# Performance work log

Hardware: AMD Instinct MI355X
Metric: run time of the kernel (lower is better)

## Reference

```python
import jax, jax.numpy as jnp
import numpy as np

FP8_MAX = 448.0  # max finite value of float8_e4m3fn


def _fp8_quant_dequant(t, scale):
    """Per-tensor static FP8 e4m3fn quantize -> dequantize (simulated real quant)."""
    q = jnp.clip(t / scale, -FP8_MAX, FP8_MAX).astype(jnp.float8_e4m3fn)
    return q.astype(jnp.float32) * scale


def setup_inputs() -> dict:
    key = jax.random.key(0)
    k1, k2, k3 = jax.random.split(key, 3)
    M, K, N = 4096, 4096, 14336  # tokens, in_features, out_features
    x = jax.random.normal(k1, (M, K), jnp.float32)
    weight = jax.random.normal(k2, (N, K), jnp.float32) * 0.02
    bias = jax.random.normal(k3, (N,), jnp.float32) * 0.01
    # static per-tensor calibration scales (amax / fp8_max)
    input_scale = (jnp.max(jnp.abs(x)) / FP8_MAX).reshape(1)
    weight_scale = (jnp.max(jnp.abs(weight)) / FP8_MAX).reshape(1)
    return {"x": x, "weight": weight, "bias": bias,
            "input_scale": input_scale, "weight_scale": weight_scale}


def reference(x, weight, bias, input_scale, weight_scale):
    # QParamsLinear forward: statically quantize input to fp8 e4m3fn with the
    # input quantizer's per-tensor scale, dequantize the fp8 weight with its
    # per-tensor scale, run the GEMM (y = x_dq @ W_dq^T), and add bias.
    s_in = input_scale[0]
    s_w = weight_scale[0]
    x_dq = _fp8_quant_dequant(x, s_in)      # [M, K]
    w_dq = _fp8_quant_dequant(weight, s_w)  # [N, K]
    return jnp.einsum('mk,nk->mn', x_dq, w_dq) + bias[None, :]
```

## Files before the change

kernel.cpp:

```cpp
#include <hip/hip_runtime.h>
#include <stdint.h>

typedef float f32x4 __attribute__((ext_vector_type(4)));
typedef int   i32x8 __attribute__((ext_vector_type(8)));
typedef long  i64x2 __attribute__((ext_vector_type(2)));

#define FP8_MAX_V 448.0f

__device__ __forceinline__ uint32_t pack4_fp8(float a, float b, float c, float d) {
    a = fminf(fmaxf(a, -FP8_MAX_V), FP8_MAX_V);
    b = fminf(fmaxf(b, -FP8_MAX_V), FP8_MAX_V);
    c = fminf(fmaxf(c, -FP8_MAX_V), FP8_MAX_V);
    d = fminf(fmaxf(d, -FP8_MAX_V), FP8_MAX_V);
    int v = 0;
    v = __builtin_amdgcn_cvt_pk_fp8_f32(a, b, v, false);
    v = __builtin_amdgcn_cvt_pk_fp8_f32(c, d, v, true);
    return (uint32_t)v;
}

__global__ void quant_fp8_kernel(const float* __restrict__ in,
                                 uint32_t* __restrict__ out,
                                 const float* __restrict__ scale_ptr,
                                 long long n4) {
    const float s = scale_ptr[0];
    long long i = (long long)blockIdx.x * blockDim.x + threadIdx.x;
    const long long stride = (long long)gridDim.x * blockDim.x;
    const float4* in4 = (const float4*)in;
    for (; i < n4; i += stride) {
        float4 v = in4[i];
        out[i] = pack4_fp8(v.x / s, v.y / s, v.z / s, v.w / s);
    }
}

__global__ __launch_bounds__(256, 2) void gemm_mxfp8_kernel(
    const uint8_t* __restrict__ qA,
    const uint8_t* __restrict__ qB,
    const float* __restrict__ bias,
    const float* __restrict__ s_in_p,
    const float* __restrict__ s_w_p,
    float* __restrict__ C,
    int M, int N, int K) {
    __shared__ uint8_t lds[49152];

    const int tid = threadIdx.x;
    const int w   = tid >> 6;
    const int l   = tid & 63;
    const int wr  = w >> 1;
    const int wc  = w & 1;
    const int lr  = l & 15;
    const int lg  = l >> 4;
    const int lsw = lr & 7;

    const int cpx = (int)gridDim.x >> 3;
    const int swz = ((int)blockIdx.x & 7) * cpx + ((int)blockIdx.x >> 3);
    const int bm  = (swz & 15) << 8;
    const int bn  = (swz >> 4) << 7;

    const float outscale = s_in_p[0] * s_w_p[0];
    const int NT = K >> 7;

    const int off0 = (((lg << 1) ^ lsw) << 4);
    const int off1 = off0 ^ 16;

    f32x4 acc[8][4];
#pragma unroll
    for (int mi = 0; mi < 8; ++mi)
#pragma unroll
        for (int ni = 0; ni < 4; ++ni)
            acc[mi][ni] = (f32x4){0.f, 0.f, 0.f, 0.f};

    const int srow = tid >> 3;
    const int sc   = (((tid & 7) ^ (srow & 7)) << 4);
    const uint8_t* sA = qA + (size_t)(bm + srow) * K + sc;
    const uint8_t* sB = qB + (size_t)(bn + srow) * K + sc;
    const int dstw = w << 10;

    union frag { i32x8 v; i64x2 h[2]; };

    for (int kt = 0; kt < NT; ++kt) {
        const int kb = kt << 7;
#pragma unroll
        for (int i = 0; i < 8; ++i) {
            __builtin_amdgcn_global_load_lds(
                (const __attribute__((address_space(1))) void*)(sA + (size_t)(i * 32) * K + kb),
                (__attribute__((address_space(3))) void*)(lds + i * 4096 + dstw), 16, 0, 0);
        }
#pragma unroll
        for (int i = 0; i < 4; ++i) {
            __builtin_amdgcn_global_load_lds(
                (const __attribute__((address_space(1))) void*)(sB + (size_t)(i * 32) * K + kb),
                (__attribute__((address_space(3))) void*)(lds + 32768 + i * 4096 + dstw), 16, 0, 0);
        }
        __syncthreads();

        i32x8 a[8];
#pragma unroll
        for (int mi = 0; mi < 8; ++mi) {
            const uint8_t* base = lds + ((wr * 128 + mi * 16 + lr) << 7);
            frag u;
            u.h[0] = *(const i64x2*)(base + off0);
            u.h[1] = *(const i64x2*)(base + off1);
            a[mi] = u.v;
        }
#pragma unroll
        for (int ni = 0; ni < 4; ++ni) {
            const uint8_t* base = lds + 32768 + ((wc * 64 + ni * 16 + lr) << 7);
            frag u;
            u.h[0] = *(const i64x2*)(base + off0);
            u.h[1] = *(const i64x2*)(base + off1);
            const i32x8 b = u.v;
#pragma unroll
            for (int mi = 0; mi < 8; ++mi)
                acc[mi][ni] = __builtin_amdgcn_mfma_scale_f32_16x16x128_f8f6f4(
                    a[mi], b, acc[mi][ni],
                    0, 0,
                    0, 127,
                    0, 127);
        }
        asm volatile("s_waitcnt lgkmcnt(0)" ::: "memory");
        __builtin_amdgcn_sched_barrier(0);
        __builtin_amdgcn_s_barrier();
    }

    const int crow0 = bm + wr * 128 + (lg << 2);
    const int ccol0 = bn + wc * 64 + lr;
#pragma unroll
    for (int ni = 0; ni < 4; ++ni) {
        const int col = ccol0 + ni * 16;
        const float bv = bias[col];
#pragma unroll
        for (int mi = 0; mi < 8; ++mi) {
            const int row = crow0 + mi * 16;
#pragma unroll
            for (int r = 0; r < 4; ++r)
                C[(size_t)(row + r) * N + col] = acc[mi][ni][r] * outscale + bv;
        }
    }
}

extern "C" void kernel_launch(void* const* d_in, const int* in_sizes, int n_in,
                              void* d_out, int out_size, void* d_ws, size_t ws_size,
                              hipStream_t stream) {
    const float* x    = (const float*)d_in[0];
    const float* wt   = (const float*)d_in[1];
    const float* bias = (const float*)d_in[2];
    const float* s_in = (const float*)d_in[3];
    const float* s_w  = (const float*)d_in[4];
    float* out = (float*)d_out;

    const long long xe = in_sizes[0];
    const long long we = in_sizes[1];
    const int N = in_sizes[2];
    const int K = (int)(we / N);
    const int M = (int)(xe / K);

    uint8_t* qx = (uint8_t*)d_ws;
    uint8_t* qw = qx + xe;

    quant_fp8_kernel<<<2048, 256, 0, stream>>>(x,  (uint32_t*)qx, s_in, xe >> 2);
    quant_fp8_kernel<<<2048, 256, 0, stream>>>(wt, (uint32_t*)qw, s_w,  we >> 2);

    dim3 grid((M / 256) * (N / 128));
    gemm_mxfp8_kernel<<<grid, 256, 0, stream>>>(qx, qw, bias, s_in, s_w, out,
                                                M, N, K);
}
```

Before: 401.6 us.

## Double-buffer A tile in LDS and load B fragments directly into registers

The A tile is now double-buffered in LDS, so the next tile's global_load_lds is issued before the current tile's MFMAs, overlapping global latency with compute. The B operand bypasses LDS and is loaded straight from global memory into register fragments, also prefetched one tile ahead with ping-pong register buffers. This removes the per-iteration load-then-sync stall but raises register pressure. It also relies on uncoalesced direct B loads and on NT being even.

```diff
diff --git a/kernel.cpp b/kernel.cpp
--- a/kernel.cpp
+++ b/kernel.cpp
@@ -40,7 +40,7 @@
     const float* __restrict__ s_w_p,
     float* __restrict__ C,
     int M, int N, int K) {
-    __shared__ uint8_t lds[49152];
+    __shared__ uint8_t lds[2][32768];
 
     const int tid = threadIdx.x;
     const int w   = tid >> 6;
@@ -72,54 +72,63 @@
     const int srow = tid >> 3;
     const int sc   = (((tid & 7) ^ (srow & 7)) << 4);
     const uint8_t* sA = qA + (size_t)(bm + srow) * K + sc;
-    const uint8_t* sB = qB + (size_t)(bn + srow) * K + sc;
     const int dstw = w << 10;
 
+    const uint8_t* bR0 = qB + (size_t)(bn + wc * 64 +  0 + lr) * K + (lg << 5);
+    const uint8_t* bR1 = qB + (size_t)(bn + wc * 64 + 16 + lr) * K + (lg << 5);
+    const uint8_t* bR2 = qB + (size_t)(bn + wc * 64 + 32 + lr) * K + (lg << 5);
+    const uint8_t* bR3 = qB + (size_t)(bn + wc * 64 + 48 + lr) * K + (lg << 5);
+
     union frag { i32x8 v; i64x2 h[2]; };
+    frag pb0[4], pb1[4];
 
-    for (int kt = 0; kt < NT; ++kt) {
-        const int kb = kt << 7;
-#pragma unroll
-        for (int i = 0; i < 8; ++i) {
-            __builtin_amdgcn_global_load_lds(
-                (const __attribute__((address_space(1))) void*)(sA + (size_t)(i * 32) * K + kb),
-                (__attribute__((address_space(3))) void*)(lds + i * 4096 + dstw), 16, 0, 0);
-        }
-#pragma unroll
-        for (int i = 0; i < 4; ++i) {
-            __builtin_amdgcn_global_load_lds(
-                (const __attribute__((address_space(1))) void*)(sB + (size_t)(i * 32) * K + kb),
-                (__attribute__((address_space(3))) void*)(lds + 32768 + i * 4096 + dstw), 16, 0, 0);
-        }
-        __syncthreads();
+#define STAGE_A(SL, KB) do { \
+    _Pragma("unroll") \
+    for (int i = 0; i < 8; ++i) { \
+        __builtin_amdgcn_global_load_lds( \
+            (const __attribute__((address_space(1))) void*)(sA + (size_t)(i * 32) * K + (KB)), \
+            (__attribute__((address_space(3))) void*)(&lds[SL][0] + i * 4096 + dstw), 16, 0, 0); \
+    } } while (0)
 
-        i32x8 a[8];
-#pragma unroll
-        for (int mi = 0; mi < 8; ++mi) {
-            const uint8_t* base = lds + ((wr * 128 + mi * 16 + lr) << 7);
-            frag u;
-            u.h[0] = *(const i64x2*)(base + off0);
-            u.h[1] = *(const i64x2*)(base + off1);
-            a[mi] = u.v;
-        }
-#pragma unroll
-        for (int ni = 0; ni < 4; ++ni) {
-            const uint8_t* base = lds + 32768 + ((wc * 64 + ni * 16 + lr) << 7);
-            frag u;
-            u.h[0] = *(const i64x2*)(base + off0);
-            u.h[1] = *(const i64x2*)(base + off1);
-            const i32x8 b = u.v;
-#pragma unroll
-            for (int mi = 0; mi < 8; ++mi)
-                acc[mi][ni] = __builtin_amdgcn_mfma_scale_f32_16x16x128_f8f6f4(
-                    a[mi], b, acc[mi][ni],
-                    0, 0,
-                    0, 127,
-                    0, 127);
-        }
-        asm volatile("s_waitcnt lgkmcnt(0)" ::: "memory");
-        __builtin_amdgcn_sched_barrier(0);
-        __builtin_amdgcn_s_barrier();
+#define LOAD_B(BUF, KB) do { \
+    BUF[0].h[0] = *(const i64x2*)(bR0 + (KB));      BUF[0].h[1] = *(const i64x2*)(bR0 + (KB) + 16); \
+    BUF[1].h[0] = *(const i64x2*)(bR1 + (KB));      BUF[1].h[1] = *(const i64x2*)(bR1 + (KB) + 16); \
+    BUF[2].h[0] = *(const i64x2*)(bR2 + (KB));      BUF[2].h[1] = *(const i64x2*)(bR2 + (KB) + 16); \
+    BUF[3].h[0] = *(const i64x2*)(bR3 + (KB));      BUF[3].h[1] = *(const i64x2*)(bR3 + (KB) + 16); \
+} while (0)
+
+#define TILE_BODY(TT, SLOT, BCUR, BNXT) do { \
+    const int tn = ((TT) + 1 < NT) ? (TT) + 1 : 0; \
+    STAGE_A((SLOT) ^ 1, tn << 7); \
+    __builtin_amdgcn_sched_barrier(0); \
+    LOAD_B(BNXT, (size_t)tn << 7); \
+    __builtin_amdgcn_sched_barrier(0); \
+    const uint8_t* sbase = &lds[SLOT][0]; \
+    _Pragma("unroll") \
+    for (int mi = 0; mi < 8; ++mi) { \
+        frag ua; \
+        const uint8_t* p = sbase + ((wr * 128 + mi * 16 + lr) << 7); \
+        ua.h[0] = *(const i64x2*)(p + off0); \
+        ua.h[1] = *(const i64x2*)(p + off1); \
+        _Pragma("unroll") \
+        for (int ni = 0; ni < 4; ++ni) \
+            acc[mi][ni] = __builtin_amdgcn_mfma_scale_f32_16x16x128_f8f6f4( \
+                ua.v, BCUR[ni].v, acc[mi][ni], 0, 0, 0, 127, 0, 127); \
+    } \
+    asm volatile("s_waitcnt lgkmcnt(0)" ::: "memory"); \
+    __builtin_amdgcn_sched_barrier(0); \
+    asm volatile("s_waitcnt vmcnt(8)" ::: "memory"); \
+    __builtin_amdgcn_s_barrier(); \
+} while (0)
+
+    STAGE_A(0, 0);
+    LOAD_B(pb0, 0);
+    asm volatile("s_waitcnt vmcnt(0)" ::: "memory");
+    __builtin_amdgcn_s_barrier();
+
+    for (int T = 0; T < NT; T += 2) {
+        TILE_BODY(T,     0, pb0, pb1);
+        TILE_BODY(T + 1, 1, pb1, pb0);
     }
 
     const int crow0 = bm + wr * 128 + (lg << 2);
@@ -136,6 +145,9 @@
                 C[(size_t)(row + r) * N + col] = acc[mi][ni][r] * outscale + bv;
         }
     }
+#undef STAGE_A
+#undef LOAD_B
+#undef TILE_BODY
 }
 
 extern "C" void kernel_launch(void* const* d_in, const int* in_sizes, int n_in,
```

Result: slower. 442.1 us, median of 2 (+10.1%).
